# Kernel tuning notes

Hardware: AMD Instinct MI355X
Metric: run time of the kernel (lower is better)

## Reference

```python
import jax, jax.numpy as jnp
import numpy as np

N_HEAD = 16


def setup_inputs() -> dict:
    key = jax.random.key(0)
    ks = jax.random.split(key, 5)
    B, T, C = 4, 2048, 1024
    s = 1.0 / np.sqrt(C)
    x = jax.random.normal(ks[0], (B, T, C), dtype=jnp.float32)
    wq = jax.random.normal(ks[1], (C, C), dtype=jnp.float32) * s
    wk = jax.random.normal(ks[2], (C, C), dtype=jnp.float32) * s
    wv = jax.random.normal(ks[3], (C, C), dtype=jnp.float32) * s
    wo = jax.random.normal(ks[4], (C, C), dtype=jnp.float32) * s
    return {"x": x, "wq": wq, "wk": wk, "wv": wv, "wo": wo}


def _attn(x, wq, wk, wv, wo):
    B, T, C = x.shape
    H = N_HEAD
    D = C // H
    scale = 1.0 / np.sqrt(D)
    # nn.Linear(x) = x @ W.T; weights stored as [out, in]
    q = (x @ wq.T).reshape(B, T, H, D).transpose(0, 2, 1, 3)  # [B,H,T,D]
    k = (x @ wk.T).reshape(B, T, H, D).transpose(0, 2, 1, 3)
    v = (x @ wv.T).reshape(B, T, H, D).transpose(0, 2, 1, 3)
    scores = jnp.einsum("bhtd,bhsd->bhts", q, k) * scale  # [B,H,T,T]
    mask = jnp.triu(jnp.full((T, T), -jnp.inf, dtype=scores.dtype), k=1)
    attn = jax.nn.softmax(scores + mask, axis=-1)
    out = jnp.einsum("bhts,bhsd->bhtd", attn, v)  # [B,H,T,D]
    out = out.transpose(0, 2, 1, 3).reshape(B, T, C)
    return out @ wo.T


def reference(x, wq, wk, wv, wo):
    return _attn(x, wq, wk, wv, wo)
```

## Files before the change

### kernel.cpp

```cpp
#include <hip/hip_runtime.h>

typedef __bf16 bf16x8 __attribute__((ext_vector_type(8)));
typedef float f32x4 __attribute__((ext_vector_type(4)));
typedef unsigned short ushortx8 __attribute__((ext_vector_type(8)));
typedef unsigned short ushortx4 __attribute__((ext_vector_type(4)));

#if __has_builtin(__builtin_amdgcn_exp2f)
#define EXP2F(x) __builtin_amdgcn_exp2f(x)
#else
#define EXP2F(x) exp2f(x)
#endif
#if __has_builtin(__builtin_amdgcn_rcpf)
#define RCPF(x) __builtin_amdgcn_rcpf(x)
#else
#define RCPF(x) (1.0f / (x))
#endif

__device__ __forceinline__ unsigned short f2bf(float f) {
    unsigned int u = __builtin_bit_cast(unsigned int, f);
    u += 0x7fffu + ((u >> 16) & 1u);
    return (unsigned short)(u >> 16);
}

__device__ __forceinline__ bf16x8 ld_frag(const unsigned short* p) {
    return __builtin_bit_cast(bf16x8, *(const ushortx8*)p);
}

__device__ __forceinline__ unsigned int pack_bf2(float lo, float hi) {
#if __has_builtin(__builtin_amdgcn_cvt_pk_bf16_f32)
    typedef __bf16 bf16x2 __attribute__((ext_vector_type(2)));
    bf16x2 v = __builtin_amdgcn_cvt_pk_bf16_f32(lo, hi);
    return __builtin_bit_cast(unsigned int, v);
#else
    unsigned int ulo = __builtin_bit_cast(unsigned int, lo) + 0x8000u;
    unsigned int uhi = __builtin_bit_cast(unsigned int, hi) + 0x8000u;
    return __builtin_amdgcn_perm(uhi, ulo, 0x07060302u);
#endif
}

__device__ __forceinline__ void async_cp16(const unsigned short* g, unsigned short* l) {
    __builtin_amdgcn_global_load_lds(
        (const __attribute__((address_space(1))) unsigned int*)g,
        (__attribute__((address_space(3))) unsigned int*)(unsigned long)(unsigned long long)(uintptr_t)
            reinterpret_cast<uintptr_t>(l),
        16, 0, 0);
}

__global__ void cvt_kernel(const float* __restrict__ src, unsigned short* __restrict__ dst, int n4) {
    int i = blockIdx.x * blockDim.x + threadIdx.x;
    if (i < n4) {
        float4 f = ((const float4*)src)[i];
        ushortx4 u = { f2bf(f.x), f2bf(f.y), f2bf(f.z), f2bf(f.w) };
        ((ushortx4*)dst)[i] = u;
    }
}

__global__ void cvt4_kernel(const float* __restrict__ s0, const float* __restrict__ s1,
                            const float* __restrict__ s2, const float* __restrict__ s3,
                            unsigned short* __restrict__ dst) {
    const float* src = (blockIdx.y == 0) ? s0 : (blockIdx.y == 1) ? s1 : (blockIdx.y == 2) ? s2 : s3;
    unsigned short* d = dst + (size_t)blockIdx.y * (1024 * 1024);
    int i = blockIdx.x * blockDim.x + threadIdx.x;
    float4 f = ((const float4*)src)[i];
    ushortx4 u = { f2bf(f.x), f2bf(f.y), f2bf(f.z), f2bf(f.w) };
    ((ushortx4*)d)[i] = u;
}

__global__ __launch_bounds__(256, 2) void qkv_gemm(
    const unsigned short* __restrict__ xb,
    const unsigned short* __restrict__ wqb,
    const unsigned short* __restrict__ wkb,
    const unsigned short* __restrict__ wvb,
    unsigned short* __restrict__ q_ws,
    unsigned short* __restrict__ k_ws,
    unsigned short* __restrict__ v_ws)
{
    __shared__ __align__(16) unsigned short A_lds[128 * 32];
    __shared__ __align__(16) unsigned short B_lds[128 * 32];

    const int tid = threadIdx.x;
    const int wv = tid >> 6;
    const int lane = tid & 63;
    const int quad = lane >> 4;
    const int l15 = lane & 15;
    const int wm = wv >> 1;
    const int wn = wv & 1;

    const int m0 = blockIdx.x * 128;
    const int mat = blockIdx.y >> 3;
    const int n0 = (blockIdx.y & 7) * 128;
    const unsigned short* wb = (mat == 0) ? wqb : (mat == 1 ? wkb : wvb);

    const int srow = lane >> 2;
    const int scol = (lane & 3) * 8;
    const unsigned short* ag0 = xb + (size_t)(m0 + wv * 32 + srow) * 1024 + scol;
    const unsigned short* ag1 = ag0 + 16 * 1024;
    const unsigned short* bg0 = wb + (size_t)(n0 + wv * 32 + srow) * 1024 + scol;
    const unsigned short* bg1 = bg0 + 16 * 1024;
    unsigned short* la0 = A_lds + (wv * 32) * 32;
    unsigned short* la1 = A_lds + (wv * 32 + 16) * 32;
    unsigned short* lb0 = B_lds + (wv * 32) * 32;
    unsigned short* lb1 = B_lds + (wv * 32 + 16) * 32;

    f32x4 acc[4][4] = {};

    for (int kt = 0; kt < 1024; kt += 32) {
        __syncthreads();
        async_cp16(ag0 + kt, la0);
        async_cp16(ag1 + kt, la1);
        async_cp16(bg0 + kt, lb0);
        async_cp16(bg1 + kt, lb1);
        __builtin_amdgcn_s_waitcnt(0x0F70);
        __syncthreads();

        bf16x8 af[4], bf[4];
#pragma unroll
        for (int i = 0; i < 4; ++i)
            af[i] = ld_frag(A_lds + (wm * 64 + i * 16 + l15) * 32 + quad * 8);
#pragma unroll
        for (int i = 0; i < 4; ++i)
            bf[i] = ld_frag(B_lds + (wn * 64 + i * 16 + l15) * 32 + quad * 8);
#pragma unroll
        for (int i = 0; i < 4; ++i)
#pragma unroll
            for (int j = 0; j < 4; ++j)
                acc[i][j] = __builtin_amdgcn_mfma_f32_16x16x32_bf16(af[i], bf[j], acc[i][j], 0, 0, 0);
    }

    const float qscale = 0.125f * 1.4426950408889634f;
    const int mbase = m0 + wm * 64;
    const int nbase = n0 + wn * 64;
#pragma unroll
    for (int i = 0; i < 4; ++i) {
        const int mrow = mbase + i * 16 + quad * 4;
        const int b = mrow >> 11;
        const int trow = mrow & 2047;
#pragma unroll
        for (int j = 0; j < 4; ++j) {
            const int nloc = nbase + j * 16 + l15;
            const int h = nloc >> 6, d = nloc & 63;
            if (mat == 2) {
                ushortx4 pk = { f2bf(acc[i][j][0]), f2bf(acc[i][j][1]),
                                f2bf(acc[i][j][2]), f2bf(acc[i][j][3]) };
                *(ushortx4*)&v_ws[(((size_t)(b * 16 + h)) * 64 + d) * 2048 + trow] = pk;
            } else {
                unsigned short* dst = (mat == 0) ? q_ws : k_ws;
                float sc = (mat == 0) ? qscale : 1.0f;
                size_t base = (((size_t)(b * 16 + h)) * 2048 + trow) * 64 + d;
                dst[base]       = f2bf(acc[i][j][0] * sc);
                dst[base + 64]  = f2bf(acc[i][j][1] * sc);
                dst[base + 128] = f2bf(acc[i][j][2] * sc);
                dst[base + 192] = f2bf(acc[i][j][3] * sc);
            }
        }
    }
}

__global__ __launch_bounds__(256, 2) void attn_kernel(
    const unsigned short* __restrict__ q_ws,
    const unsigned short* __restrict__ k_ws,
    const unsigned short* __restrict__ v_ws,
    unsigned short* __restrict__ o_ws)
{
    __shared__ __align__(16) unsigned short K_lds[128][72];
    __shared__ __align__(16) unsigned short Vt_lds[64][136];
    __shared__ __align__(16) unsigned short P_lds[128][136];

    const int tid = threadIdx.x;
    const int wvid = tid >> 6, lane = tid & 63, quad = lane >> 4, l15 = lane & 15;
    const int bh = blockIdx.x;
    const int b = bh >> 4, h = bh & 15;
    const int bt = 15 - (int)blockIdx.y;
    const int t0 = bt * 128;

    const unsigned short* qb = q_ws + (size_t)bh * 2048 * 64;
    const unsigned short* kb = k_ws + (size_t)bh * 2048 * 64;
    const unsigned short* vb = v_ws + (size_t)bh * 64 * 2048;

    ushortx8 ones_u = { 0x3F80, 0x3F80, 0x3F80, 0x3F80, 0x3F80, 0x3F80, 0x3F80, 0x3F80 };
    const bf16x8 ones = __builtin_bit_cast(bf16x8, ones_u);

    bf16x8 bq[2][2];
#pragma unroll
    for (int it = 0; it < 2; ++it)
#pragma unroll
        for (int kk = 0; kk < 2; ++kk)
            bq[it][kk] = ld_frag(qb + (size_t)(t0 + wvid * 32 + it * 16 + l15) * 64 + kk * 32 + quad * 8);

    f32x4 acc_o[2][4] = {};
    f32x4 l_acc[2] = {};

    const int kr = tid >> 1, kc = (tid & 1) * 32;
    const int vr = tid >> 2, vc = (tid & 3) * 32;

    for (int j = 0; j <= bt; ++j) {
        const int s0 = j * 128;
        ushortx8 kvr[4], vvr[4];
#pragma unroll
        for (int u = 0; u < 4; ++u)
            kvr[u] = *(const ushortx8*)(kb + (size_t)(s0 + kr) * 64 + kc + u * 8);
#pragma unroll
        for (int u = 0; u < 4; ++u)
            vvr[u] = *(const ushortx8*)(vb + (size_t)vr * 2048 + s0 + vc + u * 8);
        __syncthreads();
#pragma unroll
        for (int u = 0; u < 4; ++u) *(ushortx8*)&K_lds[kr][kc + u * 8] = kvr[u];
#pragma unroll
        for (int u = 0; u < 4; ++u) *(ushortx8*)&Vt_lds[vr][vc + u * 8] = vvr[u];
        __syncthreads();

        f32x4 sacc[2][8] = {};
#pragma unroll
        for (int is = 0; is < 8; ++is) {
            bf16x8 k0 = ld_frag(&K_lds[is * 16 + l15][quad * 8]);
            bf16x8 k1 = ld_frag(&K_lds[is * 16 + l15][32 + quad * 8]);
            sacc[0][is] = __builtin_amdgcn_mfma_f32_16x16x32_bf16(k0, bq[0][0], sacc[0][is], 0, 0, 0);
            sacc[0][is] = __builtin_amdgcn_mfma_f32_16x16x32_bf16(k1, bq[0][1], sacc[0][is], 0, 0, 0);
            sacc[1][is] = __builtin_amdgcn_mfma_f32_16x16x32_bf16(k0, bq[1][0], sacc[1][is], 0, 0, 0);
            sacc[1][is] = __builtin_amdgcn_mfma_f32_16x16x32_bf16(k1, bq[1][1], sacc[1][is], 0, 0, 0);
        }

        if (j == bt) {
#pragma unroll
            for (int it = 0; it < 2; ++it) {
                const int tl = wvid * 32 + it * 16 + l15;
#pragma unroll
                for (int is = 0; is < 8; ++is)
#pragma unroll
                    for (int r = 0; r < 4; ++r) {
                        const int sl = is * 16 + quad * 4 + r;
                        if (sl > tl) sacc[it][is][r] = -1.0e30f;
                    }
            }
        }

#pragma unroll
        for (int it = 0; it < 2; ++it) {
            const int row = wvid * 32 + it * 16 + l15;
#pragma unroll
            for (int is = 0; is < 8; ++is) {
                float p0 = EXP2F(sacc[it][is][0]);
                float p1 = EXP2F(sacc[it][is][1]);
                float p2 = EXP2F(sacc[it][is][2]);
                float p3 = EXP2F(sacc[it][is][3]);
                uint2 pk = { pack_bf2(p0, p1), pack_bf2(p2, p3) };
                *(uint2*)&P_lds[row][is * 16 + quad * 4] = pk;
            }
        }

        __threadfence_block();

#pragma unroll
        for (int kk = 0; kk < 4; ++kk) {
            bf16x8 p0 = ld_frag(&P_lds[wvid * 32 + l15][kk * 32 + quad * 8]);
            bf16x8 p1 = ld_frag(&P_lds[wvid * 32 + 16 + l15][kk * 32 + quad * 8]);
            l_acc[0] = __builtin_amdgcn_mfma_f32_16x16x32_bf16(p0, ones, l_acc[0], 0, 0, 0);
            l_acc[1] = __builtin_amdgcn_mfma_f32_16x16x32_bf16(p1, ones, l_acc[1], 0, 0, 0);
#pragma unroll
            for (int id = 0; id < 4; ++id) {
                bf16x8 bv = ld_frag(&Vt_lds[id * 16 + l15][kk * 32 + quad * 8]);
                acc_o[0][id] = __builtin_amdgcn_mfma_f32_16x16x32_bf16(p0, bv, acc_o[0][id], 0, 0, 0);
                acc_o[1][id] = __builtin_amdgcn_mfma_f32_16x16x32_bf16(p1, bv, acc_o[1][id], 0, 0, 0);
            }
        }
    }

#pragma unroll
    for (int it = 0; it < 2; ++it) {
        f32x4 rinv;
#pragma unroll
        for (int r = 0; r < 4; ++r) rinv[r] = RCPF(l_acc[it][r]);
#pragma unroll
        for (int id = 0; id < 4; ++id)
#pragma unroll
            for (int r = 0; r < 4; ++r) {
                int tg = t0 + wvid * 32 + it * 16 + quad * 4 + r;
                int c = h * 64 + id * 16 + l15;
                o_ws[(size_t)(b * 2048 + tg) * 1024 + c] = f2bf(acc_o[it][id][r] * rinv[r]);
            }
    }
}

__global__ __launch_bounds__(256, 2) void out_gemm(
    const unsigned short* __restrict__ ob,
    const unsigned short* __restrict__ wob,
    float* __restrict__ out)
{
    __shared__ __align__(16) unsigned short A_lds[128 * 32];
    __shared__ __align__(16) unsigned short B_lds[128 * 32];

    const int tid = threadIdx.x;
    const int wv = tid >> 6;
    const int lane = tid & 63;
    const int quad = lane >> 4;
    const int l15 = lane & 15;
    const int wm = wv >> 1;
    const int wn = wv & 1;

    const int m0 = blockIdx.x * 128;
    const int n0 = blockIdx.y * 128;

    const int srow = lane >> 2;
    const int scol = (lane & 3) * 8;
    const unsigned short* ag0 = ob + (size_t)(m0 + wv * 32 + srow) * 1024 + scol;
    const unsigned short* ag1 = ag0 + 16 * 1024;
    const unsigned short* bg0 = wob + (size_t)(n0 + wv * 32 + srow) * 1024 + scol;
    const unsigned short* bg1 = bg0 + 16 * 1024;
    unsigned short* la0 = A_lds + (wv * 32) * 32;
    unsigned short* la1 = A_lds + (wv * 32 + 16) * 32;
    unsigned short* lb0 = B_lds + (wv * 32) * 32;
    unsigned short* lb1 = B_lds + (wv * 32 + 16) * 32;

    f32x4 acc[4][4] = {};

    for (int kt = 0; kt < 1024; kt += 32) {
        __syncthreads();
        async_cp16(ag0 + kt, la0);
        async_cp16(ag1 + kt, la1);
        async_cp16(bg0 + kt, lb0);
        async_cp16(bg1 + kt, lb1);
        __builtin_amdgcn_s_waitcnt(0x0F70);
        __syncthreads();

        bf16x8 af[4], bf[4];
#pragma unroll
        for (int i = 0; i < 4; ++i)
            af[i] = ld_frag(A_lds + (wm * 64 + i * 16 + l15) * 32 + quad * 8);
#pragma unroll
        for (int i = 0; i < 4; ++i)
            bf[i] = ld_frag(B_lds + (wn * 64 + i * 16 + l15) * 32 + quad * 8);
#pragma unroll
        for (int i = 0; i < 4; ++i)
#pragma unroll
            for (int j = 0; j < 4; ++j)
                acc[i][j] = __builtin_amdgcn_mfma_f32_16x16x32_bf16(af[i], bf[j], acc[i][j], 0, 0, 0);
    }

    const int mbase = m0 + wm * 64;
    const int nbase = n0 + wn * 64;
#pragma unroll
    for (int i = 0; i < 4; ++i) {
        const int mrow = mbase + i * 16 + quad * 4;
#pragma unroll
        for (int j = 0; j < 4; ++j) {
            const int ncol = nbase + j * 16 + l15;
            float* dst = out + (size_t)mrow * 1024 + ncol;
            dst[0]        = acc[i][j][0];
            dst[1024]     = acc[i][j][1];
            dst[2048]     = acc[i][j][2];
            dst[3072]     = acc[i][j][3];
        }
    }
}

extern "C" void kernel_launch(void* const* d_in, const int* in_sizes, int n_in,
                              void* d_out, int out_size, void* d_ws, size_t ws_size,
                              hipStream_t stream) {
    const float* x  = (const float*)d_in[0];
    const float* wq = (const float*)d_in[1];
    const float* wk = (const float*)d_in[2];
    const float* wv = (const float*)d_in[3];
    const float* wo = (const float*)d_in[4];
    float* out = (float*)d_out;

    unsigned short* ws = (unsigned short*)d_ws;
    unsigned short* xb   = ws;
    unsigned short* wqb  = xb  + (size_t)8192 * 1024;
    unsigned short* wkb  = wqb + (size_t)1024 * 1024;
    unsigned short* wvb  = wkb + (size_t)1024 * 1024;
    unsigned short* wob  = wvb + (size_t)1024 * 1024;
    unsigned short* q_ws = wob + (size_t)1024 * 1024;
    unsigned short* k_ws = q_ws + (size_t)8192 * 1024;
    unsigned short* v_ws = k_ws + (size_t)8192 * 1024;
    unsigned short* o_ws = v_ws + (size_t)8192 * 1024;

    int n4 = (8192 * 1024) / 4;
    cvt_kernel<<<(n4 + 255) / 256, 256, 0, stream>>>(x, xb, n4);
    cvt4_kernel<<<dim3(1024, 4), 256, 0, stream>>>(wq, wk, wv, wo, wqb);

    qkv_gemm<<<dim3(64, 24), 256, 0, stream>>>(xb, wqb, wkb, wvb, q_ws, k_ws, v_ws);
    attn_kernel<<<dim3(64, 16), 256, 0, stream>>>(q_ws, k_ws, v_ws, o_ws);
    out_gemm<<<dim3(64, 8), 256, 0, stream>>>(o_ws, wob, out);
}
```

Baseline: 235.3 us.

## Swizzle GEMM LDS tiles and stream attention K/V fragments straight from global

In both projection GEMMs, the column chunk each lane copies into LDS is rotated by row, and the fragment reads use the matching rotation, to spread LDS bank accesses. In the attention kernel, K and V are no longer staged through shared memory: each wave loads its MFMA fragments directly from global memory. This removes the staging stores and both block barriers per tile, and the smaller LDS footprint allows three blocks per CU instead of two. The cost is that each wave re-reads K/V that the other waves also read, which raises L2/global traffic and exposes load latency with no explicit prefetch.

```diff
diff --git a/kernel.cpp b/kernel.cpp
--- a/kernel.cpp
+++ b/kernel.cpp
@@ -92,7 +92,7 @@
     const unsigned short* wb = (mat == 0) ? wqb : (mat == 1 ? wkb : wvb);
 
     const int srow = lane >> 2;
-    const int scol = (lane & 3) * 8;
+    const int scol = ((((lane & 3) - ((lane >> 3) & 3)) & 3) * 8);
     const unsigned short* ag0 = xb + (size_t)(m0 + wv * 32 + srow) * 1024 + scol;
     const unsigned short* ag1 = ag0 + 16 * 1024;
     const unsigned short* bg0 = wb + (size_t)(n0 + wv * 32 + srow) * 1024 + scol;
@@ -102,6 +102,8 @@
     unsigned short* lb0 = B_lds + (wv * 32) * 32;
     unsigned short* lb1 = B_lds + (wv * 32 + 16) * 32;
 
+    const int fcol = ((quad + (l15 >> 1)) & 3) * 8;
+
     f32x4 acc[4][4] = {};
 
     for (int kt = 0; kt < 1024; kt += 32) {
@@ -116,10 +118,10 @@
         bf16x8 af[4], bf[4];
 #pragma unroll
         for (int i = 0; i < 4; ++i)
-            af[i] = ld_frag(A_lds + (wm * 64 + i * 16 + l15) * 32 + quad * 8);
-#pragma unroll
-        for (int i = 0; i < 4; ++i)
-            bf[i] = ld_frag(B_lds + (wn * 64 + i * 16 + l15) * 32 + quad * 8);
+            af[i] = ld_frag(A_lds + (wm * 64 + i * 16 + l15) * 32 + fcol);
+#pragma unroll
+        for (int i = 0; i < 4; ++i)
+            bf[i] = ld_frag(B_lds + (wn * 64 + i * 16 + l15) * 32 + fcol);
 #pragma unroll
         for (int i = 0; i < 4; ++i)
 #pragma unroll
@@ -156,15 +158,13 @@
     }
 }
 
-__global__ __launch_bounds__(256, 2) void attn_kernel(
+__global__ __launch_bounds__(256, 3) void attn_kernel(
     const unsigned short* __restrict__ q_ws,
     const unsigned short* __restrict__ k_ws,
     const unsigned short* __restrict__ v_ws,
     unsigned short* __restrict__ o_ws)
 {
-    __shared__ __align__(16) unsigned short K_lds[128][72];
-    __shared__ __align__(16) unsigned short Vt_lds[64][136];
-    __shared__ __align__(16) unsigned short P_lds[128][136];
+    __shared__ __align__(16) unsigned short P_lds[128][138];
 
     const int tid = threadIdx.x;
     const int wvid = tid >> 6, lane = tid & 63, quad = lane >> 4, l15 = lane & 15;
@@ -190,30 +190,17 @@
     f32x4 acc_o[2][4] = {};
     f32x4 l_acc[2] = {};
 
-    const int kr = tid >> 1, kc = (tid & 1) * 32;
-    const int vr = tid >> 2, vc = (tid & 3) * 32;
+    const unsigned short* krow = kb + (size_t)l15 * 64 + quad * 8;
+    const unsigned short* vrow = vb + (size_t)l15 * 2048 + quad * 8;
 
     for (int j = 0; j <= bt; ++j) {
         const int s0 = j * 128;
-        ushortx8 kvr[4], vvr[4];
-#pragma unroll
-        for (int u = 0; u < 4; ++u)
-            kvr[u] = *(const ushortx8*)(kb + (size_t)(s0 + kr) * 64 + kc + u * 8);
-#pragma unroll
-        for (int u = 0; u < 4; ++u)
-            vvr[u] = *(const ushortx8*)(vb + (size_t)vr * 2048 + s0 + vc + u * 8);
-        __syncthreads();
-#pragma unroll
-        for (int u = 0; u < 4; ++u) *(ushortx8*)&K_lds[kr][kc + u * 8] = kvr[u];
-#pragma unroll
-        for (int u = 0; u < 4; ++u) *(ushortx8*)&Vt_lds[vr][vc + u * 8] = vvr[u];
-        __syncthreads();
 
         f32x4 sacc[2][8] = {};
 #pragma unroll
         for (int is = 0; is < 8; ++is) {
-            bf16x8 k0 = ld_frag(&K_lds[is * 16 + l15][quad * 8]);
-            bf16x8 k1 = ld_frag(&K_lds[is * 16 + l15][32 + quad * 8]);
+            bf16x8 k0 = ld_frag(krow + (size_t)(s0 + is * 16) * 64);
+            bf16x8 k1 = ld_frag(krow + (size_t)(s0 + is * 16) * 64 + 32);
             sacc[0][is] = __builtin_amdgcn_mfma_f32_16x16x32_bf16(k0, bq[0][0], sacc[0][is], 0, 0, 0);
             sacc[0][is] = __builtin_amdgcn_mfma_f32_16x16x32_bf16(k1, bq[0][1], sacc[0][is], 0, 0, 0);
             sacc[1][is] = __builtin_amdgcn_mfma_f32_16x16x32_bf16(k0, bq[1][0], sacc[1][is], 0, 0, 0);
@@ -258,7 +245,7 @@
             l_acc[1] = __builtin_amdgcn_mfma_f32_16x16x32_bf16(p1, ones, l_acc[1], 0, 0, 0);
 #pragma unroll
             for (int id = 0; id < 4; ++id) {
-                bf16x8 bv = ld_frag(&Vt_lds[id * 16 + l15][kk * 32 + quad * 8]);
+                bf16x8 bv = ld_frag(vrow + (size_t)(id * 16) * 2048 + s0 + kk * 32);
                 acc_o[0][id] = __builtin_amdgcn_mfma_f32_16x16x32_bf16(p0, bv, acc_o[0][id], 0, 0, 0);
                 acc_o[1][id] = __builtin_amdgcn_mfma_f32_16x16x32_bf16(p1, bv, acc_o[1][id], 0, 0, 0);
             }
@@ -301,7 +288,7 @@
     const int n0 = blockIdx.y * 128;
 
     const int srow = lane >> 2;
-    const int scol = (lane & 3) * 8;
+    const int scol = ((((lane & 3) - ((lane >> 3) & 3)) & 3) * 8);
     const unsigned short* ag0 = ob + (size_t)(m0 + wv * 32 + srow) * 1024 + scol;
     const unsigned short* ag1 = ag0 + 16 * 1024;
     const unsigned short* bg0 = wob + (size_t)(n0 + wv * 32 + srow) * 1024 + scol;
@@ -311,6 +298,8 @@
     unsigned short* lb0 = B_lds + (wv * 32) * 32;
     unsigned short* lb1 = B_lds + (wv * 32 + 16) * 32;
 
+    const int fcol = ((quad + (l15 >> 1)) & 3) * 8;
+
     f32x4 acc[4][4] = {};
 
     for (int kt = 0; kt < 1024; kt += 32) {
@@ -325,10 +314,10 @@
         bf16x8 af[4], bf[4];
 #pragma unroll
         for (int i = 0; i < 4; ++i)
-            af[i] = ld_frag(A_lds + (wm * 64 + i * 16 + l15) * 32 + quad * 8);
-#pragma unroll
-        for (int i = 0; i < 4; ++i)
-            bf[i] = ld_frag(B_lds + (wn * 64 + i * 16 + l15) * 32 + quad * 8);
+            af[i] = ld_frag(A_lds + (wm * 64 + i * 16 + l15) * 32 + fcol);
+#pragma unroll
+        for (int i = 0; i < 4; ++i)
+            bf[i] = ld_frag(B_lds + (wn * 64 + i * 16 + l15) * 32 + fcol);
 #pragma unroll
         for (int i = 0; i < 4; ++i)
 #pragma unroll
```

Measured after the change: 320.0 us. 36.0% more time.
